# Optimization experiments

Measured on AMD Instinct MI355X. Metric: run time of the kernel, lower is better.

The kernel has to match this reference:

```python
import jax, jax.numpy as jnp
import numpy as np

B, T, D, U = 32, 4096, 512, 512

def setup_inputs() -> dict:
    key = jax.random.key(0)
    ks = jax.random.split(key, 8)
    s = 0.02
    return {
        "query": jax.random.normal(ks[0], (B, D), dtype=jnp.float32),
        "values": jax.random.normal(ks[1], (B, T, D), dtype=jnp.float32),
        "W1": jax.random.normal(ks[2], (D, U), dtype=jnp.float32) * s,
        "b1": jnp.zeros((U,), dtype=jnp.float32),
        "W2": jax.random.normal(ks[3], (D, U), dtype=jnp.float32) * s,
        "b2": jnp.zeros((U,), dtype=jnp.float32),
        "V": jax.random.normal(ks[4], (U, 1), dtype=jnp.float32) * s,
        "bv": jnp.zeros((1,), dtype=jnp.float32),
    }

def reference(query, values, W1, b1, W2, b2, V, bv):
    # query: [B, D] -> [B, 1, U]; values: [B, T, D] -> [B, T, U]
    q_proj = (query @ W1 + b1)[:, None, :]            # [B, 1, U]
    v_proj = values @ W2 + b2                          # [B, T, U]
    scores = jnp.tanh(q_proj + v_proj) @ V + bv        # [B, T, 1]
    attn = jax.nn.softmax(scores, axis=1)              # softmax over time axis
    context = jnp.sum(attn * values, axis=1)           # [B, D]
    return context
```

## Files before the change

### kernel.cpp

```cpp
#include <hip/hip_runtime.h>
#include <hip/hip_bf16.h>
#include <math.h>

#define B_ 32
#define T_ 4096
#define D_ 512
#define U_ 512

typedef __bf16 bf16x8 __attribute__((ext_vector_type(8)));
typedef float floatx4 __attribute__((ext_vector_type(4)));
typedef unsigned short ushortx8 __attribute__((ext_vector_type(8)));

static __device__ __forceinline__ unsigned short f2bf(float f) {
  unsigned int u = __float_as_uint(f);
  unsigned int r = (u + 0x7fffu + ((u >> 16) & 1u)) >> 16;
  return (unsigned short)r;
}

static __device__ __forceinline__ float tanh_fast(float x) {
  float e = exp2f(x * 2.88539008178f);
  return 1.0f - 2.0f * __builtin_amdgcn_rcpf(1.0f + e);
}

__global__ __launch_bounds__(256) void prep_w2t(
    const float* __restrict__ W2, unsigned short* __restrict__ W2T) {
  __shared__ float tile[32][33];
  const int bx = blockIdx.x * 32;
  const int by = blockIdx.y * 32;
  const int x = threadIdx.x;
#pragma unroll
  for (int y = threadIdx.y; y < 32; y += 8)
    tile[y][x] = W2[(size_t)(bx + y) * U_ + by + x];
  __syncthreads();
#pragma unroll
  for (int y = threadIdx.y; y < 32; y += 8)
    W2T[(size_t)(by + y) * D_ + bx + x] = f2bf(tile[x][y]);
}

__global__ __launch_bounds__(256) void qproj_kernel(
    const float* __restrict__ query, const float* __restrict__ W1,
    const float* __restrict__ b1, const float* __restrict__ b2,
    float* __restrict__ qp) {
  const int b = blockIdx.x;
  const int tid = threadIdx.x;
  __shared__ float qs[D_];
  qs[tid] = query[b * D_ + tid];
  qs[tid + 256] = query[b * D_ + tid + 256];
  __syncthreads();
  const int u0 = tid * 2;
  float ax = 0.f, ay = 0.f;
#pragma unroll 8
  for (int k = 0; k < D_; ++k) {
    const float q = qs[k];
    const float2 w = *(const float2*)&W1[(size_t)k * U_ + u0];
    ax += q * w.x;
    ay += q * w.y;
  }
  qp[b * U_ + u0] = ax + b1[u0] + b2[u0];
  qp[b * U_ + u0 + 1] = ay + b1[u0 + 1] + b2[u0 + 1];
}

__global__ __launch_bounds__(256, 2) void scores_mfma(
    const float* __restrict__ values, const unsigned short* __restrict__ W2T,
    const float* __restrict__ qp, const float* __restrict__ V,
    float* __restrict__ scores) {
  const int b = blockIdx.y;
  const int t0 = blockIdx.x * 64;
  const int tid = threadIdx.x;
  const int w = tid >> 6;
  const int lane = tid & 63;
  const int lr = lane & 15;
  const int kc = lane >> 4;
  const int no = w * 128;

  __shared__ __align__(16) unsigned short As[4 * 528];
  __shared__ float red[4][64];

  const float* vbase = values + ((size_t)b * T_ + t0) * D_;
  const int arow = tid >> 2;
  const int achk = tid & 3;

  floatx4 acc[4][8];
#pragma unroll
  for (int i = 0; i < 4; ++i)
#pragma unroll
    for (int j = 0; j < 8; ++j) acc[i][j] = (floatx4)0.f;

  for (int k0 = 0; k0 < D_; k0 += 32) {
    __syncthreads();
    {
      const float4* vp = (const float4*)&vbase[(size_t)arow * D_ + k0 + achk * 8];
      const float4 f0 = vp[0];
      const float4 f1 = vp[1];
      ushortx8 pk;
      pk[0] = f2bf(f0.x); pk[1] = f2bf(f0.y);
      pk[2] = f2bf(f0.z); pk[3] = f2bf(f0.w);
      pk[4] = f2bf(f1.x); pk[5] = f2bf(f1.y);
      pk[6] = f2bf(f1.z); pk[7] = f2bf(f1.w);
      *(ushortx8*)&As[achk * 528 + arow * 8] = pk;
    }
    __syncthreads();

    bf16x8 bfr[8];
#pragma unroll
    for (int j = 0; j < 8; ++j)
      bfr[j] = __builtin_bit_cast(
          bf16x8,
          *(const ushortx8*)&W2T[(size_t)(no + j * 16 + lr) * D_ + k0 + kc * 8]);

    bf16x8 af[4];
#pragma unroll
    for (int i = 0; i < 4; ++i)
      af[i] = __builtin_bit_cast(
          bf16x8, *(ushortx8*)&As[kc * 528 + (i * 16 + lr) * 8]);

#pragma unroll
    for (int i = 0; i < 4; ++i)
#pragma unroll
      for (int j = 0; j < 8; ++j)
        acc[i][j] = __builtin_amdgcn_mfma_f32_16x16x32_bf16(af[i], bfr[j],
                                                            acc[i][j], 0, 0, 0);
  }

  const float* qpb = qp + b * U_;
  float qv[8], vv[8];
#pragma unroll
  for (int j = 0; j < 8; ++j) {
    const int u = no + j * 16 + lr;
    qv[j] = qpb[u];
    vv[j] = V[u];
  }
  const int mrow = (lane >> 4) * 4;
#pragma unroll
  for (int i = 0; i < 4; ++i) {
#pragma unroll
    for (int r = 0; r < 4; ++r) {
      float s = 0.f;
#pragma unroll
      for (int j = 0; j < 8; ++j) s += tanh_fast(acc[i][j][r] + qv[j]) * vv[j];
      s += __shfl_xor(s, 1);
      s += __shfl_xor(s, 2);
      s += __shfl_xor(s, 4);
      s += __shfl_xor(s, 8);
      if (lr == 0) red[w][i * 16 + mrow + r] = s;
    }
  }
  __syncthreads();
  if (tid < 64)
    scores[(size_t)b * T_ + t0 + tid] =
        red[0][tid] + red[1][tid] + red[2][tid] + red[3][tid];
}

__global__ __launch_bounds__(256) void softmax_kernel(float* __restrict__ sc) {
  const int b = blockIdx.x;
  const int tid = threadIdx.x;
  __shared__ float red[256];
  float* s = sc + (size_t)b * T_;
  float v[16];
  float lmax = -1e30f;
#pragma unroll
  for (int i = 0; i < 16; ++i) {
    v[i] = s[tid + 256 * i];
    lmax = fmaxf(lmax, v[i]);
  }
  red[tid] = lmax;
  __syncthreads();
  for (int off = 128; off > 0; off >>= 1) {
    if (tid < off) red[tid] = fmaxf(red[tid], red[tid + off]);
    __syncthreads();
  }
  const float m = red[0];
  __syncthreads();
  float lsum = 0.f;
#pragma unroll
  for (int i = 0; i < 16; ++i) {
    v[i] = expf(v[i] - m);
    lsum += v[i];
  }
  red[tid] = lsum;
  __syncthreads();
  for (int off = 128; off > 0; off >>= 1) {
    if (tid < off) red[tid] += red[tid + off];
    __syncthreads();
  }
  const float inv = 1.0f / red[0];
#pragma unroll
  for (int i = 0; i < 16; ++i) s[tid + 256 * i] = v[i] * inv;
}

__global__ __launch_bounds__(256) void context_kernel(
    const float* __restrict__ values, const float* __restrict__ attn,
    float* __restrict__ out) {
  const int b = blockIdx.x;
  const int t0 = blockIdx.y * 128;
  const int tid = threadIdx.x;
  const int tx = tid & 127;
  const int ty = tid >> 7;
  __shared__ float as[128];
  __shared__ float4 red[128];
  if (tid < 128) as[tid] = attn[(size_t)b * T_ + t0 + tid];
  __syncthreads();
  const float* vb = values + ((size_t)b * T_ + t0) * D_;
  float ax = 0.f, ay = 0.f, az = 0.f, aw = 0.f;
#pragma unroll 8
  for (int t = ty; t < 128; t += 2) {
    const float a = as[t];
    const float4 v = *(const float4*)&vb[(size_t)t * D_ + tx * 4];
    ax += a * v.x;
    ay += a * v.y;
    az += a * v.z;
    aw += a * v.w;
  }
  if (ty == 1) red[tx] = make_float4(ax, ay, az, aw);
  __syncthreads();
  if (ty == 0) {
    const float4 o = red[tx];
    const int d = tx * 4;
    atomicAdd(&out[b * D_ + d],     ax + o.x);
    atomicAdd(&out[b * D_ + d + 1], ay + o.y);
    atomicAdd(&out[b * D_ + d + 2], az + o.z);
    atomicAdd(&out[b * D_ + d + 3], aw + o.w);
  }
}

extern "C" void kernel_launch(void* const* d_in, const int* in_sizes, int n_in,
                              void* d_out, int out_size, void* d_ws,
                              size_t ws_size, hipStream_t stream) {
  const float* query = (const float*)d_in[0];
  const float* values = (const float*)d_in[1];
  const float* W1 = (const float*)d_in[2];
  const float* b1 = (const float*)d_in[3];
  const float* W2 = (const float*)d_in[4];
  const float* b2 = (const float*)d_in[5];
  const float* V = (const float*)d_in[6];

  float* qp = (float*)d_ws;
  float* scores = qp + (size_t)B_ * U_;
  unsigned short* W2T = (unsigned short*)(scores + (size_t)B_ * T_);
  float* out = (float*)d_out;

  hipMemsetAsync(d_out, 0, (size_t)B_ * D_ * sizeof(float), stream);

  prep_w2t<<<dim3(16, 16), dim3(32, 8), 0, stream>>>(W2, W2T);
  qproj_kernel<<<B_, 256, 0, stream>>>(query, W1, b1, b2, qp);
  scores_mfma<<<dim3(T_ / 64, B_), 256, 0, stream>>>(values, W2T, qp, V,
                                                     scores);
  softmax_kernel<<<B_, 256, 0, stream>>>(scores);
  context_kernel<<<dim3(B_, 32), 256, 0, stream>>>(values, scores, out);
}
```

Before: 567.7 us.

## Stage full bf16 values tile in LDS and prepack W2 into MFMA fragment order

The scores kernel now loads the whole 64x512 values tile into LDS (converted to bf16, with an XOR-style rotated column layout to avoid bank conflicts) once up front, rather than 16 barrier-separated k-steps of 32. W2 is pre-packed by a new prep kernel into MFMA B-fragment order, so each lane does one coalesced 16-byte load per fragment. The reduction buffer reuses the LDS tile. This removes per-step barriers and strided W2T loads, but it raises LDS use to 64KB per block, which may lower occupancy below the launch-bounds target of 2 blocks, and it serializes load then compute with no overlap.

```diff
diff --git a/kernel.cpp b/kernel.cpp
--- a/kernel.cpp
+++ b/kernel.cpp
@@ -11,10 +11,9 @@
 typedef float floatx4 __attribute__((ext_vector_type(4)));
 typedef unsigned short ushortx8 __attribute__((ext_vector_type(8)));
 
-static __device__ __forceinline__ unsigned short f2bf(float f) {
+static __device__ __forceinline__ unsigned int f2bf(float f) {
   unsigned int u = __float_as_uint(f);
-  unsigned int r = (u + 0x7fffu + ((u >> 16) & 1u)) >> 16;
-  return (unsigned short)r;
+  return (u + 0x7fffu + ((u >> 16) & 1u)) >> 16;
 }
 
 static __device__ __forceinline__ float tanh_fast(float x) {
@@ -22,19 +21,31 @@
   return 1.0f - 2.0f * __builtin_amdgcn_rcpf(1.0f + e);
 }
 
-__global__ __launch_bounds__(256) void prep_w2t(
-    const float* __restrict__ W2, unsigned short* __restrict__ W2T) {
-  __shared__ float tile[32][33];
-  const int bx = blockIdx.x * 32;
-  const int by = blockIdx.y * 32;
-  const int x = threadIdx.x;
-#pragma unroll
-  for (int y = threadIdx.y; y < 32; y += 8)
-    tile[y][x] = W2[(size_t)(bx + y) * U_ + by + x];
-  __syncthreads();
-#pragma unroll
-  for (int y = threadIdx.y; y < 32; y += 8)
-    W2T[(size_t)(by + y) * D_ + bx + x] = f2bf(tile[x][y]);
+static __device__ __forceinline__ uint4 pack8(const float4 a, const float4 b) {
+  uint4 pk;
+  pk.x = f2bf(a.x) | (f2bf(a.y) << 16);
+  pk.y = f2bf(a.z) | (f2bf(a.w) << 16);
+  pk.z = f2bf(b.x) | (f2bf(b.y) << 16);
+  pk.w = f2bf(b.z) | (f2bf(b.w) << 16);
+  return pk;
+}
+
+__global__ __launch_bounds__(256) void prep_w2b(
+    const float* __restrict__ W2, unsigned short* __restrict__ W2B) {
+  const int s = blockIdx.x * 256 + threadIdx.x;
+  const int lane = s & 63;
+  const int frag = s >> 6;
+  const int ub = frag >> 4;
+  const int kb = frag & 15;
+  const int lr = lane & 15;
+  const int kc = lane >> 4;
+  const int u = ub * 16 + lr;
+  const int k0 = kb * 32 + kc * 8;
+  ushortx8 pk;
+#pragma unroll
+  for (int j = 0; j < 8; ++j)
+    pk[j] = (unsigned short)f2bf(W2[(size_t)(k0 + j) * U_ + u]);
+  *(ushortx8*)&W2B[(size_t)s * 8] = pk;
 }
 
 __global__ __launch_bounds__(256) void qproj_kernel(
@@ -61,7 +72,7 @@
 }
 
 __global__ __launch_bounds__(256, 2) void scores_mfma(
-    const float* __restrict__ values, const unsigned short* __restrict__ W2T,
+    const float* __restrict__ values, const unsigned short* __restrict__ W2B,
     const float* __restrict__ qp, const float* __restrict__ V,
     float* __restrict__ scores) {
   const int b = blockIdx.y;
@@ -71,14 +82,22 @@
   const int lane = tid & 63;
   const int lr = lane & 15;
   const int kc = lane >> 4;
-  const int no = w * 128;
-
-  __shared__ __align__(16) unsigned short As[4 * 528];
-  __shared__ float red[4][64];
+
+  __shared__ __align__(16) unsigned short As[64 * 512];
 
   const float* vbase = values + ((size_t)b * T_ + t0) * D_;
-  const int arow = tid >> 2;
-  const int achk = tid & 3;
+
+#pragma unroll
+  for (int p = 0; p < 16; ++p) {
+    const int m = p * 256 + tid;
+    const int r = m >> 6;
+    const int k8 = m & 63;
+    const float4 f0 = *(const float4*)&vbase[(size_t)r * D_ + k8 * 8];
+    const float4 f1 = *(const float4*)&vbase[(size_t)r * D_ + k8 * 8 + 4];
+    const int c = (k8 + r * 4) & 63;
+    *(uint4*)&As[r * 512 + c * 8] = pack8(f0, f1);
+  }
+  __syncthreads();
 
   floatx4 acc[4][8];
 #pragma unroll
@@ -86,34 +105,22 @@
 #pragma unroll
     for (int j = 0; j < 8; ++j) acc[i][j] = (floatx4)0.f;
 
-  for (int k0 = 0; k0 < D_; k0 += 32) {
-    __syncthreads();
-    {
-      const float4* vp = (const float4*)&vbase[(size_t)arow * D_ + k0 + achk * 8];
-      const float4 f0 = vp[0];
-      const float4 f1 = vp[1];
-      ushortx8 pk;
-      pk[0] = f2bf(f0.x); pk[1] = f2bf(f0.y);
-      pk[2] = f2bf(f0.z); pk[3] = f2bf(f0.w);
-      pk[4] = f2bf(f1.x); pk[5] = f2bf(f1.y);
-      pk[6] = f2bf(f1.z); pk[7] = f2bf(f1.w);
-      *(ushortx8*)&As[achk * 528 + arow * 8] = pk;
-    }
-    __syncthreads();
-
+  const ushortx8* W2Bv = (const ushortx8*)W2B;
+
+#pragma unroll 4
+  for (int ks = 0; ks < 16; ++ks) {
     bf16x8 bfr[8];
 #pragma unroll
     for (int j = 0; j < 8; ++j)
       bfr[j] = __builtin_bit_cast(
-          bf16x8,
-          *(const ushortx8*)&W2T[(size_t)(no + j * 16 + lr) * D_ + k0 + kc * 8]);
-
+          bf16x8, W2Bv[((w * 8 + j) * 16 + ks) * 64 + lane]);
     bf16x8 af[4];
 #pragma unroll
-    for (int i = 0; i < 4; ++i)
-      af[i] = __builtin_bit_cast(
-          bf16x8, *(ushortx8*)&As[kc * 528 + (i * 16 + lr) * 8]);
-
+    for (int i = 0; i < 4; ++i) {
+      const int ri = i * 16 + lr;
+      const int c = (ks * 4 + kc + ri * 4) & 63;
+      af[i] = __builtin_bit_cast(bf16x8, *(ushortx8*)&As[ri * 512 + c * 8]);
+    }
 #pragma unroll
     for (int i = 0; i < 4; ++i)
 #pragma unroll
@@ -122,6 +129,7 @@
                                                             acc[i][j], 0, 0, 0);
   }
 
+  const int no = w * 128;
   const float* qpb = qp + b * U_;
   float qv[8], vv[8];
 #pragma unroll
@@ -130,6 +138,8 @@
     qv[j] = qpb[u];
     vv[j] = V[u];
   }
+  __syncthreads();
+  float* red = (float*)As;
   const int mrow = (lane >> 4) * 4;
 #pragma unroll
   for (int i = 0; i < 4; ++i) {
@@ -142,13 +152,13 @@
       s += __shfl_xor(s, 2);
       s += __shfl_xor(s, 4);
       s += __shfl_xor(s, 8);
-      if (lr == 0) red[w][i * 16 + mrow + r] = s;
+      if (lr == 0) red[w * 64 + i * 16 + mrow + r] = s;
     }
   }
   __syncthreads();
   if (tid < 64)
     scores[(size_t)b * T_ + t0 + tid] =
-        red[0][tid] + red[1][tid] + red[2][tid] + red[3][tid];
+        red[tid] + red[64 + tid] + red[128 + tid] + red[192 + tid];
 }
 
 __global__ __launch_bounds__(256) void softmax_kernel(float* __restrict__ sc) {
@@ -236,14 +246,14 @@
 
   float* qp = (float*)d_ws;
   float* scores = qp + (size_t)B_ * U_;
-  unsigned short* W2T = (unsigned short*)(scores + (size_t)B_ * T_);
+  unsigned short* W2B = (unsigned short*)(scores + (size_t)B_ * T_);
   float* out = (float*)d_out;
 
-  hipMemsetAsync(d_out, 0, (size_t)B_ * D_ * sizeof(float), stream);
-
-  prep_w2t<<<dim3(16, 16), dim3(32, 8), 0, stream>>>(W2, W2T);
+  (void)hipMemsetAsync(d_out, 0, (size_t)B_ * D_ * sizeof(float), stream);
+
+  prep_w2b<<<128, 256, 0, stream>>>(W2, W2B);
   qproj_kernel<<<B_, 256, 0, stream>>>(query, W1, b1, b2, qp);
-  scores_mfma<<<dim3(T_ / 64, B_), 256, 0, stream>>>(values, W2T, qp, V,
+  scores_mfma<<<dim3(T_ / 64, B_), 256, 0, stream>>>(values, W2B, qp, V,
                                                      scores);
   softmax_kernel<<<B_, 256, 0, stream>>>(scores);
   context_kernel<<<dim3(B_, 32), 256, 0, stream>>>(values, scores, out);
```

Measured after the change: 519.3 us. 1.09x faster.
